# Performance work log

Measured on AMD Instinct MI355X. Metric: run time of the kernel, lower is better.

## Reference

```python
import jax, jax.numpy as jnp
import numpy as np

EPS = 1e-8
EPS12 = 1e-12
TAU = 0.2
IOU_THRESHOLD = 0.5
NEG_INF = -1e9

N, C = 8192, 1024
HID, FGD, CLSD = 256, 64, 128


def setup_inputs() -> dict:
    key = jax.random.key(0)
    ks = jax.random.split(key, 16)
    roi_feats = jax.random.normal(ks[0], (N, C), dtype=jnp.float32)
    # labels in {-1 (ignore), 0 (bg), 1..20 (classes)}
    labels = jax.random.randint(ks[1], (N,), 0, 21, dtype=jnp.int64) - 1
    ious = jax.random.uniform(ks[2], (N,), dtype=jnp.float32)
    s = 0.02
    w1f = jax.random.normal(ks[3], (HID, C), dtype=jnp.float32) * s
    b1f = jnp.zeros((HID,), dtype=jnp.float32)
    w2f = jax.random.normal(ks[4], (FGD, HID), dtype=jnp.float32) * s
    b2f = jnp.zeros((FGD,), dtype=jnp.float32)
    w1c = jax.random.normal(ks[5], (HID, C), dtype=jnp.float32) * s
    b1c = jnp.zeros((HID,), dtype=jnp.float32)
    w2c = jax.random.normal(ks[6], (CLSD, HID), dtype=jnp.float32) * s
    b2c = jnp.zeros((CLSD,), dtype=jnp.float32)
    return {"roi_feats": roi_feats, "labels": labels, "ious": ious,
            "w1f": w1f, "b1f": b1f, "w2f": w2f, "b2f": b2f,
            "w1c": w1c, "b1c": b1c, "w2c": w2c, "b2c": b2c}


def _project_normalize(x, w1, b1, w2, b2):
    h = jax.nn.relu(x @ w1.T + b1)
    z = h @ w2.T + b2
    nrm = jnp.linalg.norm(z, axis=1, keepdims=True)  # F.normalize: z / max(||z||, eps)
    return z / jnp.maximum(nrm, EPS)


def _fg_bg_loss(z_fg, fg_mask, ignore_mask, iou_weight):
    n = z_fg.shape[0]
    anchor = fg_mask & ~ignore_mask
    eye = jnp.eye(n, dtype=bool)
    # pos_mask[i,j] = fg_mask[j] & ~ignore[j], self excluded
    pos = (fg_mask & ~ignore_mask)[None, :] & ~eye  # [N,N]
    sim = (z_fg @ z_fg.T) / TAU
    sim_exp = jnp.exp(sim) * (~eye).astype(sim.dtype)
    denom = sim_exp.sum(axis=1)  # [N]
    numer = jnp.sum(jnp.exp(sim) * pos.astype(sim.dtype), axis=1)  # [N]
    n_pos = pos.sum(axis=1)
    loss_i = -jnp.log((numer + EPS) / (denom + EPS))
    valid = anchor & (n_pos > 0)
    w = iou_weight
    num = jnp.sum(jnp.where(valid, loss_i * w, 0.0))
    den = jnp.sum(jnp.where(valid, w, 0.0)) + EPS
    return num / den


def _class_supcon_loss(z_cls, labels, fg_mask, ignore_mask, iou_weight):
    n = z_cls.shape[0]
    anchor = fg_mask & ~ignore_mask
    eye = jnp.eye(n, dtype=bool)
    valid_den = ~eye & ~ignore_mask[None, :]  # [N,N]
    # pos[i,j]: same label, j not ignored, labels[j] != 0, j != i, j valid
    pos = (labels[None, :] == labels[:, None]) & ~ignore_mask[None, :] & (labels[None, :] != 0)
    pos = pos & ~eye & valid_den
    sim = (z_cls @ z_cls.T) / TAU
    logits = jnp.where(valid_den, sim, NEG_INF)
    denom_log = jax.nn.logsumexp(logits, axis=1)  # [N]
    n_pos = pos.sum(axis=1)
    sum_pos = jnp.sum(jnp.where(pos, sim, 0.0), axis=1)
    n_pos_safe = jnp.maximum(n_pos, 1).astype(sim.dtype)
    loss_i = -(sum_pos - n_pos.astype(sim.dtype) * denom_log) / n_pos_safe
    valid = anchor & (n_pos > 0) & valid_den.any(axis=1)
    w = iou_weight
    num = jnp.sum(jnp.where(valid, loss_i * w, 0.0))
    den = jnp.sum(jnp.where(valid, w, 0.0)) + EPS12
    return num / den


def reference(roi_feats, labels, ious, w1f, b1f, w2f, b2f, w1c, b1c, w2c, b2c):
    z_fg = _project_normalize(roi_feats, w1f, b1f, w2f, b2f)
    z_cls = _project_normalize(roi_feats, w1c, b1c, w2c, b2c)
    ignore_mask = labels == -1
    bg_mask = (labels == 0) & ~ignore_mask
    fg_mask = (labels > 0) & ~ignore_mask
    iou_weight = jnp.where(ious > IOU_THRESHOLD, ious, 0.0)
    loss_fg_bg = _fg_bg_loss(z_fg, fg_mask, ignore_mask, iou_weight)
    loss_supcon = _class_supcon_loss(z_cls, labels, fg_mask, ignore_mask, iou_weight)
    # loss_weights = (1.0, 1.0); stacked as [loss_fg_bg, loss_supcon]
    return jnp.stack([loss_fg_bg * 1.0, loss_supcon * 1.0])
```

## Files before the change

### kernel.cpp

```cpp
#include <hip/hip_runtime.h>
#include <hip/hip_bf16.h>
#include <math.h>

#define N_ROI 8192
#define C_IN  1024
#define HIDD  256
#define FGD   64
#define CLSD  128
#define INV_TAU 5.0f
#define SCALE_LOG2E 7.2134752f
#define LN2F 0.69314718f

using frag_ab = __attribute__((ext_vector_type(8))) short;
using f32x16  = __attribute__((ext_vector_type(16))) float;

static __device__ __forceinline__ short f32_to_bf16_bits(float f) {
  unsigned u = __builtin_bit_cast(unsigned, f);
  u = (u + 0x7FFFu + ((u >> 16) & 1u)) >> 16;
  return (short)u;
}
static __device__ __forceinline__ float bf16_bits_to_f32(short b) {
  unsigned u = ((unsigned)(unsigned short)b) << 16;
  return __builtin_bit_cast(float, u);
}
static __device__ __forceinline__ float fast_exp2(float x) {
#if __has_builtin(__builtin_amdgcn_exp2f)
  return __builtin_amdgcn_exp2f(x);
#else
  return exp2f(x);
#endif
}

__global__ __launch_bounds__(256) void pack_zero_kernel(
    const float* __restrict__ w1f, const float* __restrict__ w1c,
    const float* __restrict__ w2f, const float* __restrict__ w2c,
    short* __restrict__ W1pf, short* __restrict__ W1pc,
    short* __restrict__ W2pf, short* __restrict__ W2pc,
    float* __restrict__ accum, int* __restrict__ cnt) {
  int b = blockIdx.x;
  if (b == 280) {
    int t = threadIdx.x;
    if (t < 8) accum[t] = 0.f;
    if (t < 24) cnt[t] = 0;
    return;
  }
  const float* src; short* dst; int Ksh; int b0;
  if (b < 128)      { src = w1f; dst = W1pf; Ksh = 10; b0 = 0; }
  else if (b < 256) { src = w1c; dst = W1pc; Ksh = 10; b0 = 128; }
  else if (b < 264) { src = w2f; dst = W2pf; Ksh = 8;  b0 = 256; }
  else              { src = w2c; dst = W2pc; Ksh = 8;  b0 = 264; }
  int K = 1 << Ksh;
  int f = (b - b0) * 256 + threadIdx.x;
  int r = f >> (Ksh - 3);
  int c0 = (f & ((K >> 3) - 1)) << 3;
  float4 v0 = *(const float4*)(src + (size_t)r * K + c0);
  float4 v1 = *(const float4*)(src + (size_t)r * K + c0 + 4);
  union { short s[8]; uint4 v; } o;
  o.s[0] = f32_to_bf16_bits(v0.x); o.s[1] = f32_to_bf16_bits(v0.y);
  o.s[2] = f32_to_bf16_bits(v0.z); o.s[3] = f32_to_bf16_bits(v0.w);
  o.s[4] = f32_to_bf16_bits(v1.x); o.s[5] = f32_to_bf16_bits(v1.y);
  o.s[6] = f32_to_bf16_bits(v1.z); o.s[7] = f32_to_bf16_bits(v1.w);
  ((uint4*)dst)[(size_t)((r >> 5) * (K >> 4) + (c0 >> 4)) * 64 +
                ((c0 >> 3) & 1) * 32 + (r & 31)] = o.v;
}

template<int D>
__device__ __forceinline__ void gemm2_from_lds(
    const short* __restrict__ T2, int coff,
    const short* __restrict__ W2p, const float* __restrict__ b2,
    short* __restrict__ Zr, float* __restrict__ tii,
    short* __restrict__ T, int gt) {
  int lane = threadIdx.x & 63;
  const frag_ab* Wv = (const frag_ab*)W2p;
  constexpr int NT = D / 32;
  frag_ab a[16];
  #pragma unroll
  for (int kc = 0; kc < 16; ++kc)
    a[kc] = *(const frag_ab*)&T2[(lane & 31) * 516 + coff + kc * 16 + (lane >> 5) * 8];
  f32x16 acc[NT];
  #pragma unroll
  for (int j = 0; j < NT; ++j)
    #pragma unroll
    for (int q = 0; q < 16; ++q) acc[j][q] = 0.f;
  #pragma unroll
  for (int kc = 0; kc < 16; ++kc)
    #pragma unroll
    for (int j = 0; j < NT; ++j)
      acc[j] = __builtin_amdgcn_mfma_f32_32x32x16_bf16(a[kc], Wv[(j * 16 + kc) * 64 + lane], acc[j], 0, 0, 0);
  int c = lane & 31, h = lane >> 5;
  float bb[NT];
  #pragma unroll
  for (int j = 0; j < NT; ++j) bb[j] = b2[j * 32 + c];
  float s1[16];
  #pragma unroll
  for (int r = 0; r < 16; ++r) {
    s1[r] = 0.f;
    #pragma unroll
    for (int j = 0; j < NT; ++j) {
      float v = acc[j][r] + bb[j];
      s1[r] += v * v;
    }
  }
  #pragma unroll
  for (int r = 0; r < 16; ++r)
    #pragma unroll
    for (int m = 1; m < 32; m <<= 1) s1[r] += __shfl_xor(s1[r], m);
  float s2[16];
  #pragma unroll
  for (int r = 0; r < 16; ++r) s2[r] = 0.f;
  #pragma unroll
  for (int j = 0; j < NT; ++j) {
    int cl = j * 32 + c;
    #pragma unroll
    for (int g = 0; g < 4; ++g) {
      short q0, q1, q2, q3;
      #pragma unroll
      for (int e = 0; e < 4; ++e) {
        int r = g * 4 + e;
        float sc = 1.f / fmaxf(sqrtf(s1[r]), 1e-8f);
        short qb = f32_to_bf16_bits((acc[j][r] + bb[j]) * sc);
        float zf = bf16_bits_to_f32(qb);
        s2[r] += zf * zf;
        if (e == 0) q0 = qb; else if (e == 1) q1 = qb; else if (e == 2) q2 = qb; else q3 = qb;
      }
      *(short4*)&T[cl * 36 + 4 * h + 8 * g] = make_short4(q0, q1, q2, q3);
    }
  }
  #pragma unroll
  for (int r = 0; r < 16; ++r)
    #pragma unroll
    for (int m = 1; m < 32; m <<= 1) s2[r] += __shfl_xor(s2[r], m);
  if (c == 0) {
    #pragma unroll
    for (int r = 0; r < 16; ++r)
      tii[gt * 32 + (r & 3) + 8 * (r >> 2) + 4 * h] = s2[r];
  }
  uint4* Zv = (uint4*)Zr;
  #pragma unroll
  for (int k = 0; k < D / 16; ++k) {
    int c0 = (2 * k + h) * 8;
    union { short s[8]; uint4 u; } o;
    #pragma unroll
    for (int e = 0; e < 8; ++e) o.s[e] = T[(c0 + e) * 36 + c];
    Zv[(size_t)(gt * (D / 16) + k) * 64 + h * 32 + c] = o.u;
  }
}

__global__ __launch_bounds__(256) void fused_mlp_kernel(
    const float* __restrict__ X,
    const short* __restrict__ W1pf, const short* __restrict__ W1pc,
    const float* __restrict__ b1f, const float* __restrict__ b1c,
    const short* __restrict__ W2pf, const short* __restrict__ W2pc,
    const float* __restrict__ b2f, const float* __restrict__ b2c,
    short* __restrict__ Zrf, short* __restrict__ Zrc,
    float* __restrict__ tiif, float* __restrict__ tiic,
    const int* __restrict__ labels,
    float* __restrict__ Sfg, float* __restrict__ Pfg,
    float* __restrict__ Scls, float* __restrict__ SPc,
    float* __restrict__ pfv, float* __restrict__ nimv,
    float* __restrict__ ljmv, int* __restrict__ cnt) {
  __shared__ short stageA[2][1024];
  __shared__ short T2[32 * 516];
  __shared__ short Tw[2][128 * 36];
  int tid = threadIdx.x, lane = tid & 63, wv = tid >> 6;
  int Mb = blockIdx.x;

  if (tid < 32) {
    int i = Mb * 32 + tid;
    Sfg[i] = 0.f; Pfg[i] = 0.f; Scls[i] = 0.f; SPc[i] = 0.f;
    int l = labels[i];
    pfv[i]  = (l > 0)  ? 1.f : 0.f;
    nimv[i] = (l != -1) ? 1.f : 0.f;
    ljmv[i] = (l > 0)  ? (float)l : -7.f;
    int b = l + 1; if (b < 0) b = 0; if (b > 21) b = 21;
    atomicAdd(&cnt[b], 1);
  }

  const short* Wp = (wv >> 1) ? W1pc : W1pf;
  const float* b1 = (wv >> 1) ? b1c  : b1f;
  const uint4* Wv4 = (const uint4*)Wp;
  int arow = tid >> 3;
  int ac4  = tid & 7;
  const float* Xp = X + (size_t)(Mb * 32 + arow) * C_IN + ac4 * 4;
  int aslot = ((ac4 >> 2) * 64 + ((ac4 >> 1) & 1) * 32 + arow) * 8 + (ac4 & 1) * 4;

  float4 av;
  frag_ab breg[2][8];
  f32x16 acc[4];
  #pragma unroll
  for (int nt = 0; nt < 4; ++nt)
    #pragma unroll
    for (int q = 0; q < 16; ++q) acc[nt][q] = 0.f;

  auto loadA = [&](int c) { av = *(const float4*)(Xp + c * 32); };
  auto loadB = [&](int c, int s) {
    #pragma unroll
    for (int kci = 0; kci < 2; ++kci)
      #pragma unroll
      for (int nt = 0; nt < 4; ++nt)
        breg[s][kci * 4 + nt] =
            *(const frag_ab*)&Wv4[(size_t)(((wv & 1) * 4 + nt) * 64 + c * 2 + kci) * 64 + lane];
  };
  auto storeA = [&](int buf) {
    *(short4*)&stageA[buf][aslot] =
        make_short4(f32_to_bf16_bits(av.x), f32_to_bf16_bits(av.y),
                    f32_to_bf16_bits(av.z), f32_to_bf16_bits(av.w));
  };
  auto domfma = [&](int buf, int bank) {
    frag_ab a0 = *(const frag_ab*)&stageA[buf][(0 * 64 + lane) * 8];
    frag_ab a1 = *(const frag_ab*)&stageA[buf][(1 * 64 + lane) * 8];
    #pragma unroll
    for (int nt = 0; nt < 4; ++nt)
      acc[nt] = __builtin_amdgcn_mfma_f32_32x32x16_bf16(a0, breg[bank][nt], acc[nt], 0, 0, 0);
    #pragma unroll
    for (int nt = 0; nt < 4; ++nt)
      acc[nt] = __builtin_amdgcn_mfma_f32_32x32x16_bf16(a1, breg[bank][4 + nt], acc[nt], 0, 0, 0);
  };

  loadA(0); loadB(0, 0); storeA(0);
  __syncthreads();
  for (int c = 0; c < 32; c += 2) {
    if (c + 1 < 32) { loadA(c + 1); loadB(c + 1, 1); }
    domfma(0, 0);
    if (c + 1 < 32) storeA(1);
    __syncthreads();
    if (c + 2 < 32) { loadA(c + 2); loadB(c + 2, 0); }
    domfma(1, 1);
    if (c + 2 < 32) storeA(0);
    __syncthreads();
  }
  {
    int cl31 = lane & 31, h = lane >> 5;
    int colHead = (wv & 1) * 128;
    int gbase = (wv >> 1) * 256 + colHead;
    #pragma unroll
    for (int nt = 0; nt < 4; ++nt) {
      float bb = b1[colHead + nt * 32 + cl31];
      int gc = gbase + nt * 32 + cl31;
      #pragma unroll
      for (int q = 0; q < 16; ++q) {
        int row = (q & 3) + 8 * (q >> 2) + 4 * h;
        float x = fmaxf(acc[nt][q] + bb, 0.f);
        T2[row * 516 + gc] = f32_to_bf16_bits(x);
      }
    }
  }
  __syncthreads();

  if (wv == 0)
    gemm2_from_lds<FGD>(T2, 0,   W2pf, b2f, Zrf, tiif, Tw[0], Mb);
  else if (wv == 1)
    gemm2_from_lds<CLSD>(T2, 256, W2pc, b2c, Zrc, tiic, Tw[1], Mb);
}

template<int D, int MODE, int NJT>
__device__ __forceinline__ void loss_body(
    const short* __restrict__ Zr, const int* __restrict__ labels,
    const float* __restrict__ pfv, const float* __restrict__ nimv,
    const float* __restrict__ ljmv,
    float* __restrict__ Sg, float* __restrict__ Pg) {
  constexpr int KC = D / 16;
  int tid = threadIdx.x, lane = tid & 63, wv = tid >> 6;
  int itile = blockIdx.x * 4 + wv;
  const frag_ab* Zrv = (const frag_ab*)Zr;
  frag_ab a[KC];
  #pragma unroll
  for (int kc = 0; kc < KC; ++kc) {
    frag_ab t = Zrv[(itile * KC + kc) * 64 + lane];
    #pragma unroll
    for (int e = 0; e < 8; ++e)
      t[e] = f32_to_bf16_bits(bf16_bits_to_f32(t[e]) * SCALE_LOG2E);
    a[kc] = t;
  }
  float limf[16];
  if (MODE == 1) {
    #pragma unroll
    for (int r = 0; r < 16; ++r) {
      int row = (r & 3) + 8 * (r >> 2) + 4 * (lane >> 5);
      limf[r] = (float)labels[itile * 32 + row];
    }
  }
  float Ssum[16] = {}, Psum[16] = {};
  int jt0 = blockIdx.y * NJT;
  int jlane = lane & 31;

  #pragma unroll 2
  for (int kk = 0; kk < NJT; ++kk) {
    int jt = jt0 + kk;
    int j = jt * 32 + jlane;
    float pf = 0.f, nim = 0.f, ljm = 0.f;
    if (MODE == 0) pf = pfv[j];
    else { nim = nimv[j]; ljm = ljmv[j]; }
    f32x16 acc;
    #pragma unroll
    for (int q = 0; q < 16; ++q) acc[q] = 0.f;
    #pragma unroll
    for (int kc = 0; kc < KC; ++kc) {
      frag_ab b = Zrv[((size_t)jt * KC + kc) * 64 + lane];
      acc = __builtin_amdgcn_mfma_f32_32x32x16_bf16(a[kc], b, acc, 0, 0, 0);
    }
    #pragma unroll
    for (int rr = 0; rr < 16; ++rr) {
      float e = fast_exp2(acc[rr]);
      if (MODE == 0) {
        Ssum[rr] += e;
        Psum[rr] = fmaf(pf, e, Psum[rr]);
      } else {
        Ssum[rr] = fmaf(nim, e, Ssum[rr]);
        Psum[rr] += (limf[rr] == ljm) ? acc[rr] : 0.f;
      }
    }
  }
  #pragma unroll
  for (int r = 0; r < 16; ++r) {
    float s = Ssum[r], p = Psum[r];
    #pragma unroll
    for (int m = 1; m < 32; m <<= 1) { s += __shfl_xor(s, m); p += __shfl_xor(p, m); }
    if ((lane & 31) == 0) {
      if (MODE == 1) p *= LN2F;
      int row = (r & 3) + 8 * (r >> 2) + 4 * (lane >> 5);
      atomicAdd(&Sg[itile * 32 + row], s);
      atomicAdd(&Pg[itile * 32 + row], p);
    }
  }
}

__global__ __launch_bounds__(256, 4) void loss_kernel(
    const short* __restrict__ Zrf, const short* __restrict__ Zrc,
    const int* __restrict__ labels,
    const float* __restrict__ pfv, const float* __restrict__ nimv,
    const float* __restrict__ ljmv,
    float* __restrict__ Sfg, float* __restrict__ Pfg,
    float* __restrict__ Scls, float* __restrict__ SPc) {
  if (blockIdx.z == 0)
    loss_body<FGD, 0, 16>(Zrf, labels, pfv, nimv, ljmv, Sfg, Pfg);
  else
    loss_body<CLSD, 1, 16>(Zrc, labels, pfv, nimv, ljmv, Scls, SPc);
}

__global__ __launch_bounds__(256) void finalize_kernel(
    const float* __restrict__ Sfg, const float* __restrict__ Pfg,
    const float* __restrict__ Scls, const float* __restrict__ SPc,
    const float* __restrict__ tiif, const float* __restrict__ tiic,
    const int* __restrict__ labels, const float* __restrict__ ious,
    int* __restrict__ cnt, float* __restrict__ accum, float* __restrict__ out) {
  int i = blockIdx.x * 256 + threadIdx.x;
  int l = labels[i];
  float iv = ious[i];
  float w = (iv > 0.5f) ? iv : 0.f;
  int cntP = 0;
  #pragma unroll
  for (int b = 2; b <= 21; ++b) cntP += cnt[b];
  int cntNI = N_ROI - cnt[0];
  bool Pi = (l > 0);
  float numF = 0.f, denF = 0.f, numC = 0.f, denC = 0.f;
  float eF = __expf(INV_TAU * tiif[i]);
  float Sf = Sfg[i] - eF;
  float Pf = Pfg[i] - (Pi ? eF : 0.f);
  int nposF = cntP - (Pi ? 1 : 0);
  if (Pi && nposF > 0) {
    float lossF = logf((Sf + 1e-8f) / (Pf + 1e-8f));
    numF = lossF * w; denF = w;
  }
  float tC = INV_TAU * tiic[i];
  float eC = __expf(tC);
  float Sc = Scls[i] - ((l != -1) ? eC : 0.f);
  float SP = SPc[i] - (Pi ? tC : 0.f);
  int nposC = Pi ? (cnt[l + 1] - 1) : 0;
  bool anyv = (cntNI - ((l != -1) ? 1 : 0)) > 0;
  if (Pi && nposC > 0 && anyv) {
    float lse = logf(Sc);
    float lossC = -(SP - (float)nposC * lse) / fmaxf((float)nposC, 1.f);
    numC = lossC * w; denC = w;
  }
  float v0 = numF, v1 = denF, v2 = numC, v3 = denC;
  #pragma unroll
  for (int m = 1; m < 64; m <<= 1) {
    v0 += __shfl_xor(v0, m); v1 += __shfl_xor(v1, m);
    v2 += __shfl_xor(v2, m); v3 += __shfl_xor(v3, m);
  }
  __shared__ float red[4][4];
  int lane = threadIdx.x & 63, wid = threadIdx.x >> 6;
  if (lane == 0) { red[wid][0]=v0; red[wid][1]=v1; red[wid][2]=v2; red[wid][3]=v3; }
  __syncthreads();
  if (threadIdx.x == 0) {
    float s0=0,s1=0,s2=0,s3=0;
    for (int q = 0; q < 4; ++q) { s0+=red[q][0]; s1+=red[q][1]; s2+=red[q][2]; s3+=red[q][3]; }
    atomicAdd(&accum[0], s0); atomicAdd(&accum[1], s1);
    atomicAdd(&accum[2], s2); atomicAdd(&accum[3], s3);
    __threadfence();
    int t = atomicAdd(&cnt[22], 1);
    if (t == 31) {
      __threadfence();
      out[0] = accum[0] / (accum[1] + 1e-8f);
      out[1] = accum[2] / (accum[3] + 1e-12f);
    }
  }
}

extern "C" void kernel_launch(void* const* d_in, const int* in_sizes, int n_in,
                              void* d_out, int out_size, void* d_ws, size_t ws_size,
                              hipStream_t stream) {
  const float* X    = (const float*)d_in[0];
  const int*  labels= (const int*)d_in[1];
  const float* ious = (const float*)d_in[2];
  const float* w1f  = (const float*)d_in[3];
  const float* b1f  = (const float*)d_in[4];
  const float* w2f  = (const float*)d_in[5];
  const float* b2f  = (const float*)d_in[6];
  const float* w1c  = (const float*)d_in[7];
  const float* b1c  = (const float*)d_in[8];
  const float* w2c  = (const float*)d_in[9];
  const float* b2c  = (const float*)d_in[10];
  float* out = (float*)d_out;

  char* w = (char*)d_ws;
  short* W1pf = (short*)w;            w += 524288;
  short* W1pc = (short*)w;            w += 524288;
  short* W2pf = (short*)w;            w += 32768;
  short* W2pc = (short*)w;            w += 65536;
  short* Zrf  = (short*)w;            w += 1048576;
  short* Zrc  = (short*)w;            w += 2097152;
  float* Sfg  = (float*)w;            w += 32768;
  float* Pfg  = (float*)w;            w += 32768;
  float* Scls = (float*)w;            w += 32768;
  float* SPc  = (float*)w;            w += 32768;
  float* tiif = (float*)w;            w += 32768;
  float* tiic = (float*)w;            w += 32768;
  float* pfv  = (float*)w;            w += 32768;
  float* nimv = (float*)w;            w += 32768;
  float* ljmv = (float*)w;            w += 32768;
  float* accum= (float*)w;            w += 32;
  int*   cnt  = (int*)w;              w += 96;

  pack_zero_kernel<<<281, 256, 0, stream>>>(w1f, w1c, w2f, w2c,
                                            W1pf, W1pc, W2pf, W2pc, accum, cnt);

  fused_mlp_kernel<<<256, 256, 0, stream>>>(X, W1pf, W1pc, b1f, b1c,
                                            W2pf, W2pc, b2f, b2c,
                                            Zrf, Zrc, tiif, tiic,
                                            labels, Sfg, Pfg, Scls, SPc,
                                            pfv, nimv, ljmv, cnt);

  loss_kernel<<<dim3(64, 16, 2), 256, 0, stream>>>(Zrf, Zrc, labels, pfv, nimv, ljmv,
                                                   Sfg, Pfg, Scls, SPc);

  finalize_kernel<<<N_ROI/256, 256, 0, stream>>>(Sfg, Pfg, Scls, SPc, tiif, tiic,
                                                 labels, ious, cnt, accum, out);
}
```

Baseline: 204.9 us.

## Stage shared j-tile fragments in LDS via async global-to-LDS loads

In the loss kernel, all four waves of a block previously each read the same B fragments for their j-tiles straight from global memory. The j-tiles are now loaded cooperatively into a shared LDS buffer with global_load_lds in groups of G tiles per round. Each wave then reads its MFMA operands from LDS, which cuts redundant global and L2 traffic by a factor of four. The cost is two barriers per round with no double buffering, so load latency is no longer hidden across iterations and 16KB of LDS may reduce occupancy.

```diff
diff --git a/kernel.cpp b/kernel.cpp
--- a/kernel.cpp
+++ b/kernel.cpp
@@ -29,6 +29,11 @@
 #else
   return exp2f(x);
 #endif
+}
+static __device__ __forceinline__ void async_ld16(const short* g, short* l) {
+  __builtin_amdgcn_global_load_lds(
+      (const __attribute__((address_space(1))) unsigned int*)(g),
+      (__attribute__((address_space(3))) unsigned int*)(l), 16, 0, 0);
 }
 
 __global__ __launch_bounds__(256) void pack_zero_kernel(
@@ -253,13 +258,17 @@
     gemm2_from_lds<CLSD>(T2, 256, W2pc, b2c, Zrc, tiic, Tw[1], Mb);
 }
 
-template<int D, int MODE, int NJT>
+template<int D, int MODE, int NJT, int G>
 __device__ __forceinline__ void loss_body(
+    short* sbuf,
     const short* __restrict__ Zr, const int* __restrict__ labels,
     const float* __restrict__ pfv, const float* __restrict__ nimv,
     const float* __restrict__ ljmv,
     float* __restrict__ Sg, float* __restrict__ Pg) {
   constexpr int KC = D / 16;
+  constexpr int TS = KC * 512;
+  constexpr int RS = G * TS;
+  constexpr int ROUNDS = NJT / G;
   int tid = threadIdx.x, lane = tid & 63, wv = tid >> 6;
   int itile = blockIdx.x * 4 + wv;
   const frag_ab* Zrv = (const frag_ab*)Zr;
@@ -284,30 +293,45 @@
   int jt0 = blockIdx.y * NJT;
   int jlane = lane & 31;
 
-  #pragma unroll 2
-  for (int kk = 0; kk < NJT; ++kk) {
-    int jt = jt0 + kk;
-    int j = jt * 32 + jlane;
-    float pf = 0.f, nim = 0.f, ljm = 0.f;
-    if (MODE == 0) pf = pfv[j];
-    else { nim = nimv[j]; ljm = ljmv[j]; }
-    f32x16 acc;
-    #pragma unroll
-    for (int q = 0; q < 16; ++q) acc[q] = 0.f;
-    #pragma unroll
-    for (int kc = 0; kc < KC; ++kc) {
-      frag_ab b = Zrv[((size_t)jt * KC + kc) * 64 + lane];
-      acc = __builtin_amdgcn_mfma_f32_32x32x16_bf16(a[kc], b, acc, 0, 0, 0);
-    }
-    #pragma unroll
-    for (int rr = 0; rr < 16; ++rr) {
-      float e = fast_exp2(acc[rr]);
-      if (MODE == 0) {
-        Ssum[rr] += e;
-        Psum[rr] = fmaf(pf, e, Psum[rr]);
-      } else {
-        Ssum[rr] = fmaf(nim, e, Ssum[rr]);
-        Psum[rr] += (limf[rr] == ljm) ? acc[rr] : 0.f;
+  #pragma unroll 1
+  for (int r = 0; r < ROUNDS; ++r) {
+    __syncthreads();
+    {
+      const short* src = Zr + (size_t)(jt0 + r * G) * TS;
+      #pragma unroll
+      for (int q = 0; q < RS / 2048; ++q) {
+        int off = (q * 256 + wv * 64) * 8;
+        async_ld16(src + off + lane * 8, sbuf + off);
+      }
+    }
+    float pfb[G], nimb[G], ljmb[G];
+    #pragma unroll
+    for (int t = 0; t < G; ++t) {
+      int j = (jt0 + r * G + t) * 32 + jlane;
+      if (MODE == 0) pfb[t] = pfv[j];
+      else { nimb[t] = nimv[j]; ljmb[t] = ljmv[j]; }
+    }
+    __syncthreads();
+    #pragma unroll
+    for (int t = 0; t < G; ++t) {
+      f32x16 acc;
+      #pragma unroll
+      for (int q = 0; q < 16; ++q) acc[q] = 0.f;
+      #pragma unroll
+      for (int kc = 0; kc < KC; ++kc) {
+        frag_ab b = *(const frag_ab*)&sbuf[t * TS + kc * 512 + lane * 8];
+        acc = __builtin_amdgcn_mfma_f32_32x32x16_bf16(a[kc], b, acc, 0, 0, 0);
+      }
+      #pragma unroll
+      for (int rr = 0; rr < 16; ++rr) {
+        float e = fast_exp2(acc[rr]);
+        if (MODE == 0) {
+          Ssum[rr] += e;
+          Psum[rr] = fmaf(pfb[t], e, Psum[rr]);
+        } else {
+          Ssum[rr] = fmaf(nimb[t], e, Ssum[rr]);
+          Psum[rr] += (limf[rr] == ljmb[t]) ? acc[rr] : 0.f;
+        }
       }
     }
   }
@@ -332,10 +356,11 @@
     const float* __restrict__ ljmv,
     float* __restrict__ Sfg, float* __restrict__ Pfg,
     float* __restrict__ Scls, float* __restrict__ SPc) {
+  __shared__ __align__(16) short sbuf[8192];
   if (blockIdx.z == 0)
-    loss_body<FGD, 0, 16>(Zrf, labels, pfv, nimv, ljmv, Sfg, Pfg);
+    loss_body<FGD, 0, 16, 4>(sbuf, Zrf, labels, pfv, nimv, ljmv, Sfg, Pfg);
   else
-    loss_body<CLSD, 1, 16>(Zrc, labels, pfv, nimv, ljmv, Scls, SPc);
+    loss_body<CLSD, 1, 16, 2>(sbuf, Zrc, labels, pfv, nimv, ljmv, Scls, SPc);
 }
 
 __global__ __launch_bounds__(256) void finalize_kernel(
```

Measured after the change: 224.7 us. 9.7% more time.

## Split MLP heads across grid and fold finalize into last loss block

Applied to the files above, without the earlier changes.

The fused MLP kernel now launches a 2D grid with one head per blockIdx.y. This doubles the block count to 512, halves the per-wave accumulator and B-register footprint, and shrinks LDS use, with the intent of better occupancy and CU coverage. The separate finalize kernel is removed. Instead, the last loss_kernel block to finish, detected through an atomic counter, performs the full 8192-element reduction serially and writes the output. This saves a kernel launch and the global accumulator atomics, at the cost of one block doing a serial tail pass. Each head block now re-reads the X tile.

```diff
diff --git a/kernel.cpp b/kernel.cpp
--- a/kernel.cpp
+++ b/kernel.cpp
@@ -36,11 +36,10 @@
     const float* __restrict__ w2f, const float* __restrict__ w2c,
     short* __restrict__ W1pf, short* __restrict__ W1pc,
     short* __restrict__ W2pf, short* __restrict__ W2pc,
-    float* __restrict__ accum, int* __restrict__ cnt) {
+    int* __restrict__ cnt) {
   int b = blockIdx.x;
   if (b == 280) {
     int t = threadIdx.x;
-    if (t < 8) accum[t] = 0.f;
     if (t < 24) cnt[t] = 0;
     return;
   }
@@ -66,7 +65,7 @@
 
 template<int D>
 __device__ __forceinline__ void gemm2_from_lds(
-    const short* __restrict__ T2, int coff,
+    const short* __restrict__ T2,
     const short* __restrict__ W2p, const float* __restrict__ b2,
     short* __restrict__ Zr, float* __restrict__ tii,
     short* __restrict__ T, int gt) {
@@ -76,7 +75,7 @@
   frag_ab a[16];
   #pragma unroll
   for (int kc = 0; kc < 16; ++kc)
-    a[kc] = *(const frag_ab*)&T2[(lane & 31) * 516 + coff + kc * 16 + (lane >> 5) * 8];
+    a[kc] = *(const frag_ab*)&T2[(lane & 31) * 264 + kc * 16 + (lane >> 5) * 8];
   f32x16 acc[NT];
   #pragma unroll
   for (int j = 0; j < NT; ++j)
@@ -160,12 +159,12 @@
     float* __restrict__ pfv, float* __restrict__ nimv,
     float* __restrict__ ljmv, int* __restrict__ cnt) {
   __shared__ short stageA[2][1024];
-  __shared__ short T2[32 * 516];
-  __shared__ short Tw[2][128 * 36];
+  __shared__ short T2[32 * 264];
+  __shared__ short Tw[128 * 36];
   int tid = threadIdx.x, lane = tid & 63, wv = tid >> 6;
-  int Mb = blockIdx.x;
-
-  if (tid < 32) {
+  int Mb = blockIdx.x, head = blockIdx.y;
+
+  if (head == 0 && tid < 32) {
     int i = Mb * 32 + tid;
     Sfg[i] = 0.f; Pfg[i] = 0.f; Scls[i] = 0.f; SPc[i] = 0.f;
     int l = labels[i];
@@ -176,8 +175,8 @@
     atomicAdd(&cnt[b], 1);
   }
 
-  const short* Wp = (wv >> 1) ? W1pc : W1pf;
-  const float* b1 = (wv >> 1) ? b1c  : b1f;
+  const short* Wp = head ? W1pc : W1pf;
+  const float* b1 = head ? b1c  : b1f;
   const uint4* Wv4 = (const uint4*)Wp;
   int arow = tid >> 3;
   int ac4  = tid & 7;
@@ -185,10 +184,10 @@
   int aslot = ((ac4 >> 2) * 64 + ((ac4 >> 1) & 1) * 32 + arow) * 8 + (ac4 & 1) * 4;
 
   float4 av;
-  frag_ab breg[2][8];
-  f32x16 acc[4];
-  #pragma unroll
-  for (int nt = 0; nt < 4; ++nt)
+  frag_ab breg[2][4];
+  f32x16 acc[2];
+  #pragma unroll
+  for (int nt = 0; nt < 2; ++nt)
     #pragma unroll
     for (int q = 0; q < 16; ++q) acc[nt][q] = 0.f;
 
@@ -197,9 +196,9 @@
     #pragma unroll
     for (int kci = 0; kci < 2; ++kci)
       #pragma unroll
-      for (int nt = 0; nt < 4; ++nt)
-        breg[s][kci * 4 + nt] =
-            *(const frag_ab*)&Wv4[(size_t)(((wv & 1) * 4 + nt) * 64 + c * 2 + kci) * 64 + lane];
+      for (int nt = 0; nt < 2; ++nt)
+        breg[s][kci * 2 + nt] =
+            *(const frag_ab*)&Wv4[(size_t)((wv * 2 + nt) * 64 + c * 2 + kci) * 64 + lane];
   };
   auto storeA = [&](int buf) {
     *(short4*)&stageA[buf][aslot] =
@@ -210,11 +209,11 @@
     frag_ab a0 = *(const frag_ab*)&stageA[buf][(0 * 64 + lane) * 8];
     frag_ab a1 = *(const frag_ab*)&stageA[buf][(1 * 64 + lane) * 8];
     #pragma unroll
-    for (int nt = 0; nt < 4; ++nt)
+    for (int nt = 0; nt < 2; ++nt)
       acc[nt] = __builtin_amdgcn_mfma_f32_32x32x16_bf16(a0, breg[bank][nt], acc[nt], 0, 0, 0);
     #pragma unroll
-    for (int nt = 0; nt < 4; ++nt)
-      acc[nt] = __builtin_amdgcn_mfma_f32_32x32x16_bf16(a1, breg[bank][4 + nt], acc[nt], 0, 0, 0);
+    for (int nt = 0; nt < 2; ++nt)
+      acc[nt] = __builtin_amdgcn_mfma_f32_32x32x16_bf16(a1, breg[bank][2 + nt], acc[nt], 0, 0, 0);
   };
 
   loadA(0); loadB(0, 0); storeA(0);
@@ -231,26 +230,26 @@
   }
   {
     int cl31 = lane & 31, h = lane >> 5;
-    int colHead = (wv & 1) * 128;
-    int gbase = (wv >> 1) * 256 + colHead;
-    #pragma unroll
-    for (int nt = 0; nt < 4; ++nt) {
-      float bb = b1[colHead + nt * 32 + cl31];
-      int gc = gbase + nt * 32 + cl31;
+    #pragma unroll
+    for (int nt = 0; nt < 2; ++nt) {
+      int gc = wv * 64 + nt * 32 + cl31;
+      float bb = b1[gc];
       #pragma unroll
       for (int q = 0; q < 16; ++q) {
         int row = (q & 3) + 8 * (q >> 2) + 4 * h;
         float x = fmaxf(acc[nt][q] + bb, 0.f);
-        T2[row * 516 + gc] = f32_to_bf16_bits(x);
+        T2[row * 264 + gc] = f32_to_bf16_bits(x);
       }
     }
   }
   __syncthreads();
 
-  if (wv == 0)
-    gemm2_from_lds<FGD>(T2, 0,   W2pf, b2f, Zrf, tiif, Tw[0], Mb);
-  else if (wv == 1)
-    gemm2_from_lds<CLSD>(T2, 256, W2pc, b2c, Zrc, tiic, Tw[1], Mb);
+  if (wv == 0) {
+    if (head == 0)
+      gemm2_from_lds<FGD>(T2, W2pf, b2f, Zrf, tiif, Tw, Mb);
+    else
+      gemm2_from_lds<CLSD>(T2, W2pc, b2c, Zrc, tiic, Tw, Mb);
+  }
 }
 
 template<int D, int MODE, int NJT>
@@ -325,55 +324,63 @@
   }
 }
 
+static __device__ __forceinline__ float agent_load(const float* p) {
+  return __hip_atomic_load(p, __ATOMIC_RELAXED, __HIP_MEMORY_SCOPE_AGENT);
+}
+
 __global__ __launch_bounds__(256, 4) void loss_kernel(
     const short* __restrict__ Zrf, const short* __restrict__ Zrc,
-    const int* __restrict__ labels,
+    const int* __restrict__ labels, const float* __restrict__ ious,
     const float* __restrict__ pfv, const float* __restrict__ nimv,
     const float* __restrict__ ljmv,
     float* __restrict__ Sfg, float* __restrict__ Pfg,
-    float* __restrict__ Scls, float* __restrict__ SPc) {
+    float* __restrict__ Scls, float* __restrict__ SPc,
+    const float* __restrict__ tiif, const float* __restrict__ tiic,
+    int* __restrict__ cnt, float* __restrict__ out) {
   if (blockIdx.z == 0)
     loss_body<FGD, 0, 16>(Zrf, labels, pfv, nimv, ljmv, Sfg, Pfg);
   else
     loss_body<CLSD, 1, 16>(Zrc, labels, pfv, nimv, ljmv, Scls, SPc);
-}
-
-__global__ __launch_bounds__(256) void finalize_kernel(
-    const float* __restrict__ Sfg, const float* __restrict__ Pfg,
-    const float* __restrict__ Scls, const float* __restrict__ SPc,
-    const float* __restrict__ tiif, const float* __restrict__ tiic,
-    const int* __restrict__ labels, const float* __restrict__ ious,
-    int* __restrict__ cnt, float* __restrict__ accum, float* __restrict__ out) {
-  int i = blockIdx.x * 256 + threadIdx.x;
-  int l = labels[i];
-  float iv = ious[i];
-  float w = (iv > 0.5f) ? iv : 0.f;
+
+  __threadfence();
+  __syncthreads();
+  __shared__ int isLast;
+  if (threadIdx.x == 0)
+    isLast = (atomicAdd(&cnt[22], 1) == 2047);
+  __syncthreads();
+  if (!isLast) return;
+  __threadfence();
+
   int cntP = 0;
   #pragma unroll
   for (int b = 2; b <= 21; ++b) cntP += cnt[b];
   int cntNI = N_ROI - cnt[0];
-  bool Pi = (l > 0);
-  float numF = 0.f, denF = 0.f, numC = 0.f, denC = 0.f;
-  float eF = __expf(INV_TAU * tiif[i]);
-  float Sf = Sfg[i] - eF;
-  float Pf = Pfg[i] - (Pi ? eF : 0.f);
-  int nposF = cntP - (Pi ? 1 : 0);
-  if (Pi && nposF > 0) {
-    float lossF = logf((Sf + 1e-8f) / (Pf + 1e-8f));
-    numF = lossF * w; denF = w;
-  }
-  float tC = INV_TAU * tiic[i];
-  float eC = __expf(tC);
-  float Sc = Scls[i] - ((l != -1) ? eC : 0.f);
-  float SP = SPc[i] - (Pi ? tC : 0.f);
-  int nposC = Pi ? (cnt[l + 1] - 1) : 0;
-  bool anyv = (cntNI - ((l != -1) ? 1 : 0)) > 0;
-  if (Pi && nposC > 0 && anyv) {
-    float lse = logf(Sc);
-    float lossC = -(SP - (float)nposC * lse) / fmaxf((float)nposC, 1.f);
-    numC = lossC * w; denC = w;
-  }
-  float v0 = numF, v1 = denF, v2 = numC, v3 = denC;
+  float v0 = 0.f, v1 = 0.f, v2 = 0.f, v3 = 0.f;
+  for (int i = threadIdx.x; i < N_ROI; i += 256) {
+    int l = labels[i];
+    float iv = ious[i];
+    float w = (iv > 0.5f) ? iv : 0.f;
+    bool Pi = (l > 0);
+    float eF = __expf(INV_TAU * tiif[i]);
+    float Sf = agent_load(&Sfg[i]) - eF;
+    float Pf = agent_load(&Pfg[i]) - (Pi ? eF : 0.f);
+    int nposF = cntP - (Pi ? 1 : 0);
+    if (Pi && nposF > 0) {
+      float lossF = logf((Sf + 1e-8f) / (Pf + 1e-8f));
+      v0 += lossF * w; v1 += w;
+    }
+    float tC = INV_TAU * tiic[i];
+    float eC = __expf(tC);
+    float Sc = agent_load(&Scls[i]) - ((l != -1) ? eC : 0.f);
+    float SP = agent_load(&SPc[i]) - (Pi ? tC : 0.f);
+    int nposC = Pi ? (cnt[l + 1] - 1) : 0;
+    bool anyv = (cntNI - ((l != -1) ? 1 : 0)) > 0;
+    if (Pi && nposC > 0 && anyv) {
+      float lse = logf(Sc);
+      float lossC = -(SP - (float)nposC * lse) / fmaxf((float)nposC, 1.f);
+      v2 += lossC * w; v3 += w;
+    }
+  }
   #pragma unroll
   for (int m = 1; m < 64; m <<= 1) {
     v0 += __shfl_xor(v0, m); v1 += __shfl_xor(v1, m);
@@ -386,15 +393,8 @@
   if (threadIdx.x == 0) {
     float s0=0,s1=0,s2=0,s3=0;
     for (int q = 0; q < 4; ++q) { s0+=red[q][0]; s1+=red[q][1]; s2+=red[q][2]; s3+=red[q][3]; }
-    atomicAdd(&accum[0], s0); atomicAdd(&accum[1], s1);
-    atomicAdd(&accum[2], s2); atomicAdd(&accum[3], s3);
-    __threadfence();
-    int t = atomicAdd(&cnt[22], 1);
-    if (t == 31) {
-      __threadfence();
-      out[0] = accum[0] / (accum[1] + 1e-8f);
-      out[1] = accum[2] / (accum[3] + 1e-12f);
-    }
+    out[0] = s0 / (s1 + 1e-8f);
+    out[1] = s2 / (s3 + 1e-12f);
   }
 }
 
@@ -430,21 +430,19 @@
   float* pfv  = (float*)w;            w += 32768;
   float* nimv = (float*)w;            w += 32768;
   float* ljmv = (float*)w;            w += 32768;
-  float* accum= (float*)w;            w += 32;
   int*   cnt  = (int*)w;              w += 96;
 
   pack_zero_kernel<<<281, 256, 0, stream>>>(w1f, w1c, w2f, w2c,
-                                            W1pf, W1pc, W2pf, W2pc, accum, cnt);
-
-  fused_mlp_kernel<<<256, 256, 0, stream>>>(X, W1pf, W1pc, b1f, b1c,
+                                            W1pf, W1pc, W2pf, W2pc, cnt);
+
+  fused_mlp_kernel<<<dim3(256, 2), 256, 0, stream>>>(X, W1pf, W1pc, b1f, b1c,
                                             W2pf, W2pc, b2f, b2c,
                                             Zrf, Zrc, tiif, tiic,
                                             labels, Sfg, Pfg, Scls, SPc,
                                             pfv, nimv, ljmv, cnt);
 
-  loss_kernel<<<dim3(64, 16, 2), 256, 0, stream>>>(Zrf, Zrc, labels, pfv, nimv, ljmv,
-                                                   Sfg, Pfg, Scls, SPc);
-
-  finalize_kernel<<<N_ROI/256, 256, 0, stream>>>(Sfg, Pfg, Scls, SPc, tiif, tiic,
-                                                 labels, ious, cnt, accum, out);
-}
+  loss_kernel<<<dim3(64, 16, 2), 256, 0, stream>>>(Zrf, Zrc, labels, ious,
+                                                   pfv, nimv, ljmv,
+                                                   Sfg, Pfg, Scls, SPc,
+                                                   tiif, tiic, cnt, out);
+}
```

Measured after the change: 349.0 us. +70.3%, slower.
